# Optimization experiments

Measured on AMD Instinct MI355X. Metric: run time of the kernel, lower is better.

## Reference

```python
import jax, jax.numpy as jnp
import numpy as np

N = 50000      # nodes
E = 800000     # directed edges
GNN_DIM = 128  # node feature dim
HID = 64       # per-head hidden dim of conv1
HEADS = 2
OUT = 16       # output_dim (classes)
TEXT = 500     # tf-idf text dim
M = 10000      # masked / labeled nodes


def setup_inputs() -> dict:
    key = jax.random.key(0)
    ks = jax.random.split(key, 32)
    w = lambda k, s: jax.random.normal(k, s, jnp.float32) * 0.05
    inp = {
        'text_features': jax.random.normal(ks[0], (M, TEXT), jnp.float32),
        'x': jax.random.normal(ks[1], (N, GNN_DIM), jnp.float32),
        'edge_index': jax.random.randint(ks[2], (2, E), 0, N),
        'mask': jax.random.randint(ks[3], (M,), 0, N),
        # text MLP (Linear stored as [in, out])
        'fc1_w': w(ks[4], (TEXT, 128)), 'fc1_b': w(ks[5], (128,)),
        'fc2_w': w(ks[6], (128, 64)),  'fc2_b': w(ks[7], (64,)),
        'fc3_w': w(ks[8], (64, 16)),   'fc3_b': w(ks[9], (16,)),
        'fc4_w': w(ks[10], (16, OUT)), 'fc4_b': w(ks[11], (OUT,)),
        'sc_w': w(ks[12], (TEXT, OUT)), 'sc_b': w(ks[13], (OUT,)),
        # GATConv1: in=GNN_DIM, heads=2, out=HID, concat=True
        'W1': w(ks[14], (GNN_DIM, HEADS * HID)),
        'att_src1': w(ks[15], (HEADS, HID)), 'att_dst1': w(ks[16], (HEADS, HID)),
        'b1': w(ks[17], (HEADS * HID,)),
        # GATConv2: in=2*HID, heads=1, out=OUT, concat=False
        'W2': w(ks[18], (HEADS * HID, OUT)),
        'att_src2': w(ks[19], (1, OUT)), 'att_dst2': w(ks[20], (1, OUT)),
        'b2': w(ks[21], (OUT,)),
        # fc_final: [2*OUT, OUT]
        'fcf_w': w(ks[22], (2 * OUT, OUT)), 'fcf_b': w(ks[23], (OUT,)),
    }
    return inp


def _gat_layer(h_in, src, dst, W, a_src, a_dst, b, heads, dim, concat):
    # PyG GATConv (default negative_slope=0.2, self-loops already appended)
    n = h_in.shape[0]
    h = (h_in @ W).reshape(n, heads, dim)                      # [N,H,D]
    a_s = jnp.einsum('nhd,hd->nh', h, a_src)                   # [N,H]
    a_d = jnp.einsum('nhd,hd->nh', h, a_dst)
    e = jax.nn.leaky_relu(a_s[src] + a_d[dst], 0.2)            # [E,H]
    emax = jax.ops.segment_max(e, dst, num_segments=n)
    ex = jnp.exp(e - emax[dst])
    den = jax.ops.segment_sum(ex, dst, num_segments=n)
    alpha = ex / (den[dst] + 1e-16)                            # [E,H]
    msg = h[src] * alpha[:, :, None]                           # [E,H,D]
    out = jax.ops.segment_sum(msg, dst, num_segments=n)        # [N,H,D]
    out = out.reshape(n, heads * dim) if concat else out.mean(axis=1)
    return out + b


def reference(text_features, x, edge_index, mask,
              fc1_w, fc1_b, fc2_w, fc2_b, fc3_w, fc3_b, fc4_w, fc4_b,
              sc_w, sc_b, W1, att_src1, att_dst1, b1,
              W2, att_src2, att_dst2, b2, fcf_w, fcf_b):
    n = x.shape[0]
    loop = jnp.arange(n, dtype=edge_index.dtype)
    src = jnp.concatenate([edge_index[0], loop])
    dst = jnp.concatenate([edge_index[1], loop])

    # GNN branch
    g = jax.nn.relu(_gat_layer(x, src, dst, W1, att_src1, att_dst1, b1,
                               HEADS, HID, True))
    g = _gat_layer(g, src, dst, W2, att_src2, att_dst2, b2, 1, OUT, False)
    gnn_out = g[mask]                                          # [M,OUT]

    # text MLP branch with shortcut
    t = jax.nn.relu(text_features @ fc1_w + fc1_b)
    t = jax.nn.relu(t @ fc2_w + fc2_b)
    t = jax.nn.relu(t @ fc3_w + fc3_b)
    text_out = (t @ fc4_w + fc4_b) + (text_features @ sc_w + sc_b)  # [M,OUT]

    combined = jnp.concatenate([text_out, gnn_out], axis=1)    # [M,2*OUT]
    return jax.nn.log_softmax(combined @ fcf_w + fcf_b, axis=1)
```

## Files before the change

kernel.cpp:

```cpp
#include <hip/hip_runtime.h>
#include <hip/hip_bf16.h>
#include <cmath>

#define TEXTD 500
#define GNN_DIM 128
#define DEGP(v) ((v) << 5)

typedef __attribute__((ext_vector_type(8))) short bf16x8;
typedef __attribute__((ext_vector_type(4))) float f32x4;

__device__ __forceinline__ float bf2f(unsigned short u) {
    union { unsigned int i; float f; } cv;
    cv.i = ((unsigned int)u) << 16;
    return cv.f;
}
__device__ __forceinline__ unsigned short f2b(float x) {
    __hip_bfloat16 b = __float2bfloat16(x);
    return *reinterpret_cast<unsigned short*>(&b);
}
__device__ __forceinline__ float u2f(unsigned int u) {
    union { unsigned int i; float f; } cv; cv.i = u; return cv.f;
}
__device__ __forceinline__ bf16x8 cvt8(const float* p) {
    float4 u = *(const float4*)p;
    float4 v = *(const float4*)(p + 4);
    bf16x8 f;
    f[0] = (short)f2b(u.x); f[1] = (short)f2b(u.y);
    f[2] = (short)f2b(u.z); f[3] = (short)f2b(u.w);
    f[4] = (short)f2b(v.x); f[5] = (short)f2b(v.y);
    f[6] = (short)f2b(v.z); f[7] = (short)f2b(v.w);
    return f;
}

__global__ __launch_bounds__(256) void setup_kernel(
    int* __restrict__ deg, int N, int NB,
    const float* __restrict__ fc1_w, const float* __restrict__ sc_w,
    const float* __restrict__ W1, const float* __restrict__ W2,
    const float* __restrict__ fc2_w, const float* __restrict__ fc3_w,
    const float* __restrict__ fc4_w,
    unsigned short* __restrict__ w1cat, unsigned short* __restrict__ w1g,
    unsigned short* __restrict__ w2t, unsigned short* __restrict__ fc2t,
    unsigned short* __restrict__ fc3t, unsigned short* __restrict__ fc4t)
{
    if ((int)blockIdx.x < NB) {
        int v = blockIdx.x * 256 + threadIdx.x;
        if (v < N) deg[DEGP(v)] = 0;
        return;
    }
    int idx = (blockIdx.x - NB) * 256 + threadIdx.x;
    if (idx < 73728) {
        int n = idx >> 9, k = idx & 511;
        float v = 0.f;
        if (k < TEXTD) v = (n < 128) ? fc1_w[k * 128 + n] : sc_w[k * 16 + (n - 128)];
        w1cat[idx] = f2b(v);
    } else if (idx < 90112) {
        int j = idx - 73728;
        int n = j >> 7, k = j & 127;
        w1g[j] = f2b(W1[k * 128 + n]);
    } else if (idx < 92160) {
        int j = idx - 90112;
        int n = j >> 7, k = j & 127;
        w2t[j] = f2b(W2[k * 16 + n]);
    } else if (idx < 100352) {
        int j = idx - 92160;
        int n = j >> 7, k = j & 127;
        fc2t[j] = f2b(fc2_w[k * 64 + n]);
    } else if (idx < 101376) {
        int j = idx - 100352;
        int n = j >> 6, k = j & 63;
        fc3t[j] = f2b(fc3_w[k * 16 + n]);
    } else if (idx < 101888) {
        int j = idx - 101376;
        int n = j >> 5, k = j & 31;
        fc4t[j] = f2b((k < 16) ? fc4_w[k * 16 + n] : 0.f);
    }
}

__global__ __launch_bounds__(64) void text_mfma_kernel(
    const float* __restrict__ text, const short* __restrict__ w1cat,
    const float* __restrict__ fc1_b, const float* __restrict__ sc_b,
    const short* __restrict__ fc2t, const float* __restrict__ fc2_b,
    const short* __restrict__ fc3t, const float* __restrict__ fc3_b,
    const short* __restrict__ fc4t, const float* __restrict__ fc4_b,
    float* __restrict__ text_out, int M)
{
    __shared__ unsigned short t1b[16 * 136];
    __shared__ unsigned short t2b[16 * 72];
    __shared__ unsigned short t3b[16 * 40];
    __shared__ float tscs[16 * 16];

    const int lane = threadIdx.x;
    const int q = lane >> 4, col = lane & 15;
    const int mb = blockIdx.x * 16;
    const int arow = min(mb + col, M - 1);
    const float* ap = text + (size_t)arow * TEXTD + q * 8;

    bf16x8 afrag[16];
    #pragma unroll
    for (int ks = 0; ks < 15; ks++) afrag[ks] = cvt8(ap + ks * 32);
    {
        bf16x8 f;
        int k0 = 480 + q * 8;
        #pragma unroll
        for (int e = 0; e < 8; e++) {
            int k = k0 + e;
            f[e] = (short)((k < TEXTD) ? f2b(text[(size_t)arow * TEXTD + k]) : 0);
        }
        afrag[15] = f;
    }

    for (int nb = 0; nb < 9; nb++) {
        const short* bp = w1cat + (size_t)(nb * 16 + col) * 512 + q * 8;
        f32x4 acc = {0.f, 0.f, 0.f, 0.f};
        #pragma unroll
        for (int ks = 0; ks < 16; ks++)
            acc = __builtin_amdgcn_mfma_f32_16x16x32_bf16(afrag[ks], *(const bf16x8*)(bp + ks * 32), acc, 0, 0, 0);
        #pragma unroll
        for (int i = 0; i < 4; i++) {
            int row = q * 4 + i;
            if (nb < 8) t1b[row * 136 + nb * 16 + col] = f2b(fmaxf(acc[i] + fc1_b[nb * 16 + col], 0.f));
            else        tscs[row * 16 + col] = acc[i] + sc_b[col];
        }
    }
    __syncthreads();

    const unsigned short* a2p = t1b + col * 136 + q * 8;
    #pragma unroll
    for (int nt = 0; nt < 4; nt++) {
        const short* bp = fc2t + (nt * 16 + col) * 128 + q * 8;
        f32x4 acc = {0.f, 0.f, 0.f, 0.f};
        #pragma unroll
        for (int ks = 0; ks < 4; ks++)
            acc = __builtin_amdgcn_mfma_f32_16x16x32_bf16(
                *(const bf16x8*)(a2p + ks * 32), *(const bf16x8*)(bp + ks * 32), acc, 0, 0, 0);
        #pragma unroll
        for (int i = 0; i < 4; i++) {
            int row = q * 4 + i;
            t2b[row * 72 + nt * 16 + col] = f2b(fmaxf(acc[i] + fc2_b[nt * 16 + col], 0.f));
        }
    }
    __syncthreads();

    {
        const unsigned short* a3p = t2b + col * 72 + q * 8;
        const short* bp = fc3t + col * 64 + q * 8;
        f32x4 acc = {0.f, 0.f, 0.f, 0.f};
        #pragma unroll
        for (int ks = 0; ks < 2; ks++)
            acc = __builtin_amdgcn_mfma_f32_16x16x32_bf16(
                *(const bf16x8*)(a3p + ks * 32), *(const bf16x8*)(bp + ks * 32), acc, 0, 0, 0);
        #pragma unroll
        for (int i = 0; i < 4; i++) {
            int row = q * 4 + i;
            t3b[row * 40 + col] = f2b(fmaxf(acc[i] + fc3_b[col], 0.f));
            t3b[row * 40 + 16 + col] = 0;
        }
    }
    __syncthreads();

    {
        const unsigned short* a4p = t3b + col * 40 + q * 8;
        const short* bp = fc4t + col * 32 + q * 8;
        f32x4 acc = {0.f, 0.f, 0.f, 0.f};
        acc = __builtin_amdgcn_mfma_f32_16x16x32_bf16(
            *(const bf16x8*)a4p, *(const bf16x8*)bp, acc, 0, 0, 0);
        #pragma unroll
        for (int i = 0; i < 4; i++) {
            int row = q * 4 + i;
            int rg = mb + row;
            if (rg < M) text_out[(size_t)rg * 16 + col] = acc[i] + fc4_b[col] + tscs[row * 16 + col];
        }
    }
}

__global__ __launch_bounds__(256) void gemm_h1_kernel(
    const float* __restrict__ x, const short* __restrict__ B,
    const float* __restrict__ as1w, const float* __restrict__ ad1w,
    unsigned short* __restrict__ h1, float* __restrict__ a_s, float* __restrict__ a_d, int N)
{
    const int tid = threadIdx.x;
    const int wave = tid >> 6, lane = tid & 63;
    const int q = lane >> 4, col = lane & 15;
    const int mb = blockIdx.x * 64 + wave * 16;
    const int arow = min(mb + col, N - 1);
    const float* ap = x + (size_t)arow * 128 + q * 8;

    bf16x8 afrag[4];
    #pragma unroll
    for (int ks = 0; ks < 4; ks++) afrag[ks] = cvt8(ap + ks * 32);

    float ps0[4] = {0,0,0,0}, ps1[4] = {0,0,0,0};
    float pd0[4] = {0,0,0,0}, pd1[4] = {0,0,0,0};

    #pragma unroll
    for (int nb = 0; nb < 8; nb++) {
        const short* bp = B + (size_t)(nb * 16 + col) * 128 + q * 8;
        f32x4 acc = {0.f, 0.f, 0.f, 0.f};
        #pragma unroll
        for (int ks = 0; ks < 4; ks++)
            acc = __builtin_amdgcn_mfma_f32_16x16x32_bf16(afrag[ks], *(const bf16x8*)(bp + ks * 32), acc, 0, 0, 0);
        const int j = nb * 16 + col;
        const float asj = as1w[j], adj = ad1w[j];
        #pragma unroll
        for (int i = 0; i < 4; i++) {
            int row = mb + q * 4 + i;
            if (row < N) h1[(size_t)row * 128 + j] = f2b(acc[i]);
            if (nb < 4) { ps0[i] = fmaf(acc[i], asj, ps0[i]); pd0[i] = fmaf(acc[i], adj, pd0[i]); }
            else        { ps1[i] = fmaf(acc[i], asj, ps1[i]); pd1[i] = fmaf(acc[i], adj, pd1[i]); }
        }
    }
    #pragma unroll
    for (int i = 0; i < 4; i++) {
        float v0 = ps0[i], v1 = ps1[i], w0 = pd0[i], w1 = pd1[i];
        #pragma unroll
        for (int off = 1; off < 16; off <<= 1) {
            v0 += __shfl_xor(v0, off, 16);
            v1 += __shfl_xor(v1, off, 16);
            w0 += __shfl_xor(w0, off, 16);
            w1 += __shfl_xor(w1, off, 16);
        }
        int row = mb + q * 4 + i;
        if (col == 0 && row < N) {
            a_s[2 * row] = v0; a_s[2 * row + 1] = v1;
            a_d[2 * row] = w0; a_d[2 * row + 1] = w1;
        }
    }
}

__global__ __launch_bounds__(256) void deg_hist_kernel(
    const int* __restrict__ edst, int* __restrict__ deg, int* __restrict__ rank, int E)
{
    const int base = blockIdx.x * 1024 + threadIdx.x;
    int e0 = base;
    int e1 = base + 256;
    int e2 = base + 512;
    int e3 = base + 768;
    int d0 = (e0 < E) ? edst[e0] : -1;
    int d1 = (e1 < E) ? edst[e1] : -1;
    int d2 = (e2 < E) ? edst[e2] : -1;
    int d3 = (e3 < E) ? edst[e3] : -1;
    int r0 = (d0 >= 0) ? atomicAdd(&deg[DEGP(d0)], 1) : 0;
    int r1 = (d1 >= 0) ? atomicAdd(&deg[DEGP(d1)], 1) : 0;
    int r2 = (d2 >= 0) ? atomicAdd(&deg[DEGP(d2)], 1) : 0;
    int r3 = (d3 >= 0) ? atomicAdd(&deg[DEGP(d3)], 1) : 0;
    if (d0 >= 0) rank[e0] = r0;
    if (d1 >= 0) rank[e1] = r1;
    if (d2 >= 0) rank[e2] = r2;
    if (d3 >= 0) rank[e3] = r3;
}

__global__ __launch_bounds__(256) void part_kernel(
    const int* __restrict__ deg, int* __restrict__ bsum, int N)
{
    const int tid = threadIdx.x;
    int i = blockIdx.x * 256 + tid;
    int d = (i < N) ? deg[DEGP(i)] + 1 : 0;
    #pragma unroll
    for (int off = 32; off > 0; off >>= 1) d += __shfl_down(d, off, 64);
    __shared__ int wsum[4];
    if ((tid & 63) == 0) wsum[tid >> 6] = d;
    __syncthreads();
    if (tid == 0) bsum[blockIdx.x] = wsum[0] + wsum[1] + wsum[2] + wsum[3];
}

__global__ __launch_bounds__(256) void rowptr_kernel(
    const int* __restrict__ deg, const int* __restrict__ bsum,
    int* __restrict__ rowptr, int N, int NB)
{
    __shared__ int bsc[256];
    __shared__ int sc[256];
    const int tid = threadIdx.x;

    int bv = (tid < NB) ? bsum[tid] : 0;
    bsc[tid] = bv;
    for (int off = 1; off < 256; off <<= 1) {
        __syncthreads();
        int t = (tid >= off) ? bsc[tid - off] : 0;
        __syncthreads();
        bsc[tid] += t;
    }
    __syncthreads();
    const int base = (blockIdx.x == 0) ? 0 : bsc[blockIdx.x - 1];

    const int i = blockIdx.x * 256 + tid;
    int d = (i < N) ? deg[DEGP(i)] + 1 : 0;
    sc[tid] = d;
    for (int off = 1; off < 256; off <<= 1) {
        __syncthreads();
        int t = (tid >= off) ? sc[tid - off] : 0;
        __syncthreads();
        sc[tid] += t;
    }
    __syncthreads();
    int incl = sc[tid];
    if (i < N) rowptr[i] = base + incl - d;
    if (i == N - 1) rowptr[N] = base + incl;
}

__device__ __forceinline__ float edge_w(float e) {
    return __expf(e > 0.f ? e : 0.2f * e);
}

__global__ __launch_bounds__(256) void fillw_kernel(
    const int* __restrict__ esrc, const int* __restrict__ edst,
    const int* __restrict__ rank, const int* __restrict__ rowptr,
    uint2* __restrict__ eslot,
    const float* __restrict__ a_s, const float* __restrict__ a_d, int E, int N)
{
    int e = blockIdx.x * 256 + threadIdx.x;
    if (e < E) {
        int src = esrc[e], dst = edst[e];
        int pos = rowptr[dst] + 1 + rank[e];
        float2 as = *(const float2*)(a_s + 2 * src);
        float2 ad = *(const float2*)(a_d + 2 * dst);
        unsigned int w0 = f2b(edge_w(as.x + ad.x));
        unsigned int w1 = f2b(edge_w(as.y + ad.y));
        uint2 o; o.x = (unsigned int)src; o.y = (w1 << 16) | w0;
        eslot[pos] = o;
    } else if (e < E + N) {
        int v = e - E;
        float2 as = *(const float2*)(a_s + 2 * v);
        float2 ad = *(const float2*)(a_d + 2 * v);
        unsigned int w0 = f2b(edge_w(as.x + ad.x));
        unsigned int w1 = f2b(edge_w(as.y + ad.y));
        uint2 o; o.x = (unsigned int)v; o.y = (w1 << 16) | w0;
        eslot[rowptr[v]] = o;
    }
}

template<int B>
__device__ __forceinline__ void gat1_batch(
    int i0, int end, int endm1, int wsh,
    const uint2* __restrict__ eslot, const uint2* __restrict__ h1u, unsigned int dp,
    float& a0, float& a1, float& a2, float& a3, float& den)
{
    int ics[B];
    uint2 sl[B];
    float wv[B];
    uint2 hv[B];
    #pragma unroll
    for (int k = 0; k < B; k++) ics[k] = min(i0 + 2 * k, endm1);
    #pragma unroll
    for (int k = 0; k < B; k++) sl[k] = eslot[ics[k]];
    #pragma unroll
    for (int k = 0; k < B; k++) {
        float w = u2f((sl[k].y << wsh) & 0xffff0000u);
        wv[k] = (i0 + 2 * k < end) ? w : 0.f;
    }
    #pragma unroll
    for (int k = 0; k < B; k++) hv[k] = h1u[(sl[k].x << 5) | dp];
    #pragma unroll
    for (int k = 0; k < B; k++) {
        float w = wv[k];
        den += w;
        a0 = fmaf(w, u2f(hv[k].x << 16),          a0);
        a1 = fmaf(w, u2f(hv[k].x & 0xffff0000u),  a1);
        a2 = fmaf(w, u2f(hv[k].y << 16),          a2);
        a3 = fmaf(w, u2f(hv[k].y & 0xffff0000u),  a3);
    }
}

__global__ __launch_bounds__(256) void gat1_gather_kernel(
    const int* __restrict__ rowptr, const uint2* __restrict__ eslot,
    const uint2* __restrict__ h1u,
    const float* __restrict__ b1, uint2* __restrict__ g1b, int N)
{
    const int v = blockIdx.x * 4 + (threadIdx.x >> 6);
    if (v >= N) return;
    const int lane = threadIdx.x & 63;
    const int slot = lane >> 5;
    const unsigned int dp = lane & 31;
    const int head = dp >> 4;
    const int wsh = head ? 0 : 16;
    const int beg = rowptr[v], end = rowptr[v + 1];
    const int deg = end - beg;
    const int endm1 = end - 1;
    const int i0 = beg + slot;

    float a0 = 0.f, a1 = 0.f, a2 = 0.f, a3 = 0.f, den = 0.f;

    if (deg <= 8) {
        gat1_batch<4>(i0, end, endm1, wsh, eslot, h1u, dp, a0, a1, a2, a3, den);
    } else {
        gat1_batch<8>(i0, end, endm1, wsh, eslot, h1u, dp, a0, a1, a2, a3, den);
        for (int base = i0 + 16; base < end; base += 8)
            gat1_batch<4>(base, end, endm1, wsh, eslot, h1u, dp, a0, a1, a2, a3, den);
    }

    a0 += __shfl_xor(a0, 32, 64);
    a1 += __shfl_xor(a1, 32, 64);
    a2 += __shfl_xor(a2, 32, 64);
    a3 += __shfl_xor(a3, 32, 64);
    den += __shfl_xor(den, 32, 64);

    if (lane < 32) {
        float inv = 1.f / (den + 1e-16f);
        float4 bv = *(const float4*)(b1 + 4 * dp);
        float o0 = fmaxf(fmaf(a0, inv, bv.x), 0.f);
        float o1 = fmaxf(fmaf(a1, inv, bv.y), 0.f);
        float o2 = fmaxf(fmaf(a2, inv, bv.z), 0.f);
        float o3 = fmaxf(fmaf(a3, inv, bv.w), 0.f);
        uint2 o;
        o.x = ((unsigned int)f2b(o1) << 16) | f2b(o0);
        o.y = ((unsigned int)f2b(o3) << 16) | f2b(o2);
        g1b[((unsigned int)v << 5) | dp] = o;
    }
}

__global__ __launch_bounds__(256) void gat2_proj_kernel(
    const unsigned short* __restrict__ g1b, const short* __restrict__ w2t,
    const float* __restrict__ as2w, const float* __restrict__ ad2w,
    float* __restrict__ h2, float* __restrict__ a_s2, float* __restrict__ a_d2, int N)
{
    const int tid = threadIdx.x;
    const int wave = tid >> 6, lane = tid & 63;
    const int q = lane >> 4, col = lane & 15;
    const int mb = blockIdx.x * 64 + wave * 16;
    const int arow = min(mb + col, N - 1);
    const short* ap = (const short*)g1b + (size_t)arow * 128 + q * 8;
    const short* bp = w2t + (size_t)col * 128 + q * 8;

    f32x4 acc = {0.f, 0.f, 0.f, 0.f};
    #pragma unroll
    for (int ks = 0; ks < 4; ks++)
        acc = __builtin_amdgcn_mfma_f32_16x16x32_bf16(
            *(const bf16x8*)(ap + ks * 32), *(const bf16x8*)(bp + ks * 32), acc, 0, 0, 0);

    const float asj = as2w[col], adj = ad2w[col];
    #pragma unroll
    for (int i = 0; i < 4; i++) {
        int row = mb + q * 4 + i;
        float ps = acc[i] * asj, pd = acc[i] * adj;
        #pragma unroll
        for (int off = 1; off < 16; off <<= 1) {
            ps += __shfl_xor(ps, off, 16);
            pd += __shfl_xor(pd, off, 16);
        }
        if (row < N) {
            h2[(size_t)row * 16 + col] = acc[i];
            if (col == 0) { a_s2[row] = ps; a_d2[row] = pd; }
        }
    }
}

__global__ __launch_bounds__(256) void gat2_final_kernel(
    const int* __restrict__ rowptr, const uint2* __restrict__ eslot,
    const float* __restrict__ h2,
    const float* __restrict__ a_s2, const float* __restrict__ a_d2,
    const float* __restrict__ b2, const int* __restrict__ mask,
    const float* __restrict__ text_out,
    const float* __restrict__ fcf_w, const float* __restrict__ fcf_b,
    float* __restrict__ out, int M)
{
    const int tid = threadIdx.x;
    const int m = blockIdx.x * 4 + (tid >> 6);
    if (m >= M) return;
    const int lane = tid & 63, slot = lane >> 4, c = lane & 15;
    const int v = mask[m];
    const float adv = a_d2[v];
    const int beg = rowptr[v], end = rowptr[v + 1];
    const int i0 = beg + slot;

    float acc = 0.f, den = 0.f;
    unsigned int idxs[8];
    float msk[8], as_[8], hval[8];
    #pragma unroll
    for (int k = 0; k < 8; k++) {
        int i = i0 + 4 * k;
        int ic = min(i, end - 1);
        idxs[k] = eslot[ic].x;
        msk[k] = (i < end) ? 1.f : 0.f;
    }
    #pragma unroll
    for (int k = 0; k < 8; k++) as_[k] = a_s2[idxs[k]];
    #pragma unroll
    for (int k = 0; k < 8; k++) hval[k] = h2[(idxs[k] << 4) | (unsigned)c];
    #pragma unroll
    for (int k = 0; k < 8; k++) {
        float e = as_[k] + adv;
        float w = msk[k] * __expf(e > 0.f ? e : 0.2f * e);
        den += w;
        acc = fmaf(w, hval[k], acc);
    }
    for (int i = i0 + 32; i < end; i += 4) {
        unsigned int src = eslot[i].x;
        float e = a_s2[src] + adv;
        float w = __expf(e > 0.f ? e : 0.2f * e);
        den += w;
        acc = fmaf(w, h2[(src << 4) | (unsigned)c], acc);
    }

    acc += __shfl_xor(acc, 16, 64);
    acc += __shfl_xor(acc, 32, 64);
    den += __shfl_xor(den, 16, 64);
    den += __shfl_xor(den, 32, 64);

    if (slot == 0) {
        float gval = acc / (den + 1e-16f) + b2[c];
        float tval = text_out[(size_t)m * 16 + c];

        float logit = fcf_b[c];
        #pragma unroll
        for (int k = 0; k < 16; k++) {
            logit = fmaf(__shfl(tval, k, 16), fcf_w[k * 16 + c], logit);
            logit = fmaf(__shfl(gval, k, 16), fcf_w[(16 + k) * 16 + c], logit);
        }
        float mx = logit;
        #pragma unroll
        for (int off = 8; off > 0; off >>= 1) mx = fmaxf(mx, __shfl_xor(mx, off, 16));
        float se = expf(logit - mx);
        #pragma unroll
        for (int off = 8; off > 0; off >>= 1) se += __shfl_xor(se, off, 16);
        out[(size_t)m * 16 + c] = logit - mx - logf(se);
    }
}

extern "C" void kernel_launch(void* const* d_in, const int* in_sizes, int n_in,
                              void* d_out, int out_size, void* d_ws, size_t ws_size,
                              hipStream_t stream)
{
    const float* text  = (const float*)d_in[0];
    const float* x     = (const float*)d_in[1];
    const int*   ei    = (const int*)  d_in[2];
    const int*   mask  = (const int*)  d_in[3];
    const float* fc1_w = (const float*)d_in[4];  const float* fc1_b = (const float*)d_in[5];
    const float* fc2_w = (const float*)d_in[6];  const float* fc2_b = (const float*)d_in[7];
    const float* fc3_w = (const float*)d_in[8];  const float* fc3_b = (const float*)d_in[9];
    const float* fc4_w = (const float*)d_in[10]; const float* fc4_b = (const float*)d_in[11];
    const float* sc_w  = (const float*)d_in[12]; const float* sc_b  = (const float*)d_in[13];
    const float* W1    = (const float*)d_in[14];
    const float* as1w  = (const float*)d_in[15]; const float* ad1w  = (const float*)d_in[16];
    const float* b1    = (const float*)d_in[17];
    const float* W2    = (const float*)d_in[18];
    const float* as2w  = (const float*)d_in[19]; const float* ad2w  = (const float*)d_in[20];
    const float* b2    = (const float*)d_in[21];
    const float* fcf_w = (const float*)d_in[22]; const float* fcf_b = (const float*)d_in[23];

    const int M  = in_sizes[3];
    const int N  = in_sizes[1] / GNN_DIM;
    const int E  = in_sizes[2] / 2;
    const int EP = E + N;
    const int* esrc = ei;
    const int* edst = ei + E;

    const int Np = ((N + 63) / 64) * 64;
    const int NB = (N + 255) / 256;

    float* ws = (float*)d_ws;
    size_t off = 0;
    auto alloc = [&](size_t n) { float* p = ws + off; off += (n + 63) & ~size_t(63); return p; };

    unsigned short* h1    = (unsigned short*)alloc((size_t)Np * 64);
    unsigned int*   g1b   = (unsigned int*)  alloc((size_t)N * 64);
    unsigned short* w1cat = (unsigned short*)alloc(144 * 256);
    unsigned short* w1g   = (unsigned short*)alloc(128 * 64);
    unsigned short* w2t   = (unsigned short*)alloc(16 * 64);
    unsigned short* fc2t  = (unsigned short*)alloc(64 * 64);
    unsigned short* fc3t  = (unsigned short*)alloc(16 * 32);
    unsigned short* fc4t  = (unsigned short*)alloc(16 * 16);
    float* a_s1     = alloc((size_t)2 * N);
    float* a_d1     = alloc((size_t)2 * N);
    float* h2       = alloc((size_t)N * 16);
    float* a_s2     = alloc(N);
    float* a_d2     = alloc(N);
    float* text_out = alloc((size_t)M * 16);
    uint2* eslot    = (uint2*)alloc((size_t)2 * EP);
    int* deg        = (int*)alloc((size_t)N * 32);
    int* rank       = (int*)alloc(E);
    int* rowptr     = (int*)alloc(N + 1);
    int* bsum       = (int*)alloc(256);

    const int convBlocks = (101888 + 255) / 256;

    setup_kernel<<<NB + convBlocks, 256, 0, stream>>>(
        deg, N, NB, fc1_w, sc_w, W1, W2, fc2_w, fc3_w, fc4_w,
        w1cat, w1g, w2t, fc2t, fc3t, fc4t);

    deg_hist_kernel<<<(E + 1023) / 1024, 256, 0, stream>>>(edst, deg, rank, E);
    part_kernel<<<NB, 256, 0, stream>>>(deg, bsum, N);
    rowptr_kernel<<<NB, 256, 0, stream>>>(deg, bsum, rowptr, N, NB);

    gemm_h1_kernel<<<Np / 64, 256, 0, stream>>>(
        x, (const short*)w1g, as1w, ad1w, h1, a_s1, a_d1, N);

    fillw_kernel<<<(E + N + 255) / 256, 256, 0, stream>>>(
        esrc, edst, rank, rowptr, eslot, a_s1, a_d1, E, N);

    text_mfma_kernel<<<(M + 15) / 16, 64, 0, stream>>>(
        text, (const short*)w1cat, fc1_b, sc_b,
        (const short*)fc2t, fc2_b, (const short*)fc3t, fc3_b,
        (const short*)fc4t, fc4_b, text_out, M);

    gat1_gather_kernel<<<(N + 3) / 4, 256, 0, stream>>>(
        rowptr, eslot, (const uint2*)h1, b1, (uint2*)g1b, N);

    gat2_proj_kernel<<<Np / 64, 256, 0, stream>>>(
        (const unsigned short*)g1b, (const short*)w2t, as2w, ad2w, h2, a_s2, a_d2, N);

    gat2_final_kernel<<<(M + 3) / 4, 256, 0, stream>>>(
        rowptr, eslot, h2, a_s2, a_d2, b2, mask, text_out, fcf_w, fcf_b,
        (float*)d_out, M);
}
```

Before: 182.0 us.

## Split text MLP first-layer K dimension across four waves with LDS reduction

The text MLP kernel moves from one wave per 16-row tile to four waves. Each wave computes a partial product over a 128-wide slice of the 500-dim input, and the partials are reduced through shared memory. The fc2 layer is then split across waves by output tile, while fc3 and fc4 run on wave 0 only. This cuts per-wave register pressure and serial MFMA chain length, and adds a large LDS partial buffer (about 36KB per block) plus extra barriers, which may limit occupancy.

```diff
diff --git a/kernel.cpp b/kernel.cpp
--- a/kernel.cpp
+++ b/kernel.cpp
@@ -76,7 +76,7 @@
     }
 }
 
-__global__ __launch_bounds__(64) void text_mfma_kernel(
+__global__ __launch_bounds__(256) void text_mfma_kernel(
     const float* __restrict__ text, const short* __restrict__ w1cat,
     const float* __restrict__ fc1_b, const float* __restrict__ sc_b,
     const short* __restrict__ fc2t, const float* __restrict__ fc2_b,
@@ -84,50 +84,70 @@
     const short* __restrict__ fc4t, const float* __restrict__ fc4_b,
     float* __restrict__ text_out, int M)
 {
+    __shared__ float part[4 * 9 * 256];
     __shared__ unsigned short t1b[16 * 136];
     __shared__ unsigned short t2b[16 * 72];
     __shared__ unsigned short t3b[16 * 40];
     __shared__ float tscs[16 * 16];
 
-    const int lane = threadIdx.x;
+    const int tid = threadIdx.x;
+    const int w = tid >> 6, lane = tid & 63;
     const int q = lane >> 4, col = lane & 15;
     const int mb = blockIdx.x * 16;
     const int arow = min(mb + col, M - 1);
-    const float* ap = text + (size_t)arow * TEXTD + q * 8;
-
-    bf16x8 afrag[16];
-    #pragma unroll
-    for (int ks = 0; ks < 15; ks++) afrag[ks] = cvt8(ap + ks * 32);
+    const int kofs = w * 128;
+
+    bf16x8 afrag[4];
+    #pragma unroll
+    for (int ks = 0; ks < 4; ks++) {
+        int k0 = kofs + ks * 32 + q * 8;
+        if (k0 + 7 < TEXTD) {
+            afrag[ks] = cvt8(text + (size_t)arow * TEXTD + k0);
+        } else {
+            bf16x8 f;
+            #pragma unroll
+            for (int e = 0; e < 8; e++) {
+                int k = k0 + e;
+                f[e] = (short)((k < TEXTD) ? f2b(text[(size_t)arow * TEXTD + k]) : 0);
+            }
+            afrag[ks] = f;
+        }
+    }
+
+    for (int nb = 0; nb < 9; nb++) {
+        const short* bp = w1cat + (size_t)(nb * 16 + col) * 512 + kofs + q * 8;
+        f32x4 acc = {0.f, 0.f, 0.f, 0.f};
+        #pragma unroll
+        for (int ks = 0; ks < 4; ks++)
+            acc = __builtin_amdgcn_mfma_f32_16x16x32_bf16(afrag[ks], *(const bf16x8*)(bp + ks * 32), acc, 0, 0, 0);
+        #pragma unroll
+        for (int i = 0; i < 4; i++)
+            part[w * 2304 + nb * 256 + i * 64 + lane] = acc[i];
+    }
+    __syncthreads();
+
     {
-        bf16x8 f;
-        int k0 = 480 + q * 8;
-        #pragma unroll
-        for (int e = 0; e < 8; e++) {
-            int k = k0 + e;
-            f[e] = (short)((k < TEXTD) ? f2b(text[(size_t)arow * TEXTD + k]) : 0);
-        }
-        afrag[15] = f;
-    }
-
-    for (int nb = 0; nb < 9; nb++) {
-        const short* bp = w1cat + (size_t)(nb * 16 + col) * 512 + q * 8;
-        f32x4 acc = {0.f, 0.f, 0.f, 0.f};
-        #pragma unroll
-        for (int ks = 0; ks < 16; ks++)
-            acc = __builtin_amdgcn_mfma_f32_16x16x32_bf16(afrag[ks], *(const bf16x8*)(bp + ks * 32), acc, 0, 0, 0);
-        #pragma unroll
-        for (int i = 0; i < 4; i++) {
-            int row = q * 4 + i;
-            if (nb < 8) t1b[row * 136 + nb * 16 + col] = f2b(fmaxf(acc[i] + fc1_b[nb * 16 + col], 0.f));
-            else        tscs[row * 16 + col] = acc[i] + sc_b[col];
+        int nb0 = w * 2;
+        int cnt = (w == 3) ? 3 : 2;
+        for (int t = 0; t < cnt; t++) {
+            int nb = nb0 + t;
+            #pragma unroll
+            for (int i = 0; i < 4; i++) {
+                float a = part[nb * 256 + i * 64 + lane]
+                        + part[2304 + nb * 256 + i * 64 + lane]
+                        + part[4608 + nb * 256 + i * 64 + lane]
+                        + part[6912 + nb * 256 + i * 64 + lane];
+                int row = q * 4 + i;
+                if (nb < 8) t1b[row * 136 + nb * 16 + col] = f2b(fmaxf(a + fc1_b[nb * 16 + col], 0.f));
+                else        tscs[row * 16 + col] = a + sc_b[col];
+            }
         }
     }
     __syncthreads();
 
-    const unsigned short* a2p = t1b + col * 136 + q * 8;
-    #pragma unroll
-    for (int nt = 0; nt < 4; nt++) {
-        const short* bp = fc2t + (nt * 16 + col) * 128 + q * 8;
+    {
+        const unsigned short* a2p = t1b + col * 136 + q * 8;
+        const short* bp = fc2t + (w * 16 + col) * 128 + q * 8;
         f32x4 acc = {0.f, 0.f, 0.f, 0.f};
         #pragma unroll
         for (int ks = 0; ks < 4; ks++)
@@ -136,39 +156,39 @@
         #pragma unroll
         for (int i = 0; i < 4; i++) {
             int row = q * 4 + i;
-            t2b[row * 72 + nt * 16 + col] = f2b(fmaxf(acc[i] + fc2_b[nt * 16 + col], 0.f));
+            t2b[row * 72 + w * 16 + col] = f2b(fmaxf(acc[i] + fc2_b[w * 16 + col], 0.f));
         }
     }
     __syncthreads();
 
-    {
-        const unsigned short* a3p = t2b + col * 72 + q * 8;
-        const short* bp = fc3t + col * 64 + q * 8;
-        f32x4 acc = {0.f, 0.f, 0.f, 0.f};
-        #pragma unroll
-        for (int ks = 0; ks < 2; ks++)
+    if (w == 0) {
+        {
+            const unsigned short* a3p = t2b + col * 72 + q * 8;
+            const short* bp = fc3t + col * 64 + q * 8;
+            f32x4 acc = {0.f, 0.f, 0.f, 0.f};
+            #pragma unroll
+            for (int ks = 0; ks < 2; ks++)
+                acc = __builtin_amdgcn_mfma_f32_16x16x32_bf16(
+                    *(const bf16x8*)(a3p + ks * 32), *(const bf16x8*)(bp + ks * 32), acc, 0, 0, 0);
+            #pragma unroll
+            for (int i = 0; i < 4; i++) {
+                int row = q * 4 + i;
+                t3b[row * 40 + col] = f2b(fmaxf(acc[i] + fc3_b[col], 0.f));
+                t3b[row * 40 + 16 + col] = 0;
+            }
+        }
+        {
+            const unsigned short* a4p = t3b + col * 40 + q * 8;
+            const short* bp = fc4t + col * 32 + q * 8;
+            f32x4 acc = {0.f, 0.f, 0.f, 0.f};
             acc = __builtin_amdgcn_mfma_f32_16x16x32_bf16(
-                *(const bf16x8*)(a3p + ks * 32), *(const bf16x8*)(bp + ks * 32), acc, 0, 0, 0);
-        #pragma unroll
-        for (int i = 0; i < 4; i++) {
-            int row = q * 4 + i;
-            t3b[row * 40 + col] = f2b(fmaxf(acc[i] + fc3_b[col], 0.f));
-            t3b[row * 40 + 16 + col] = 0;
-        }
-    }
-    __syncthreads();
-
-    {
-        const unsigned short* a4p = t3b + col * 40 + q * 8;
-        const short* bp = fc4t + col * 32 + q * 8;
-        f32x4 acc = {0.f, 0.f, 0.f, 0.f};
-        acc = __builtin_amdgcn_mfma_f32_16x16x32_bf16(
-            *(const bf16x8*)a4p, *(const bf16x8*)bp, acc, 0, 0, 0);
-        #pragma unroll
-        for (int i = 0; i < 4; i++) {
-            int row = q * 4 + i;
-            int rg = mb + row;
-            if (rg < M) text_out[(size_t)rg * 16 + col] = acc[i] + fc4_b[col] + tscs[row * 16 + col];
+                *(const bf16x8*)a4p, *(const bf16x8*)bp, acc, 0, 0, 0);
+            #pragma unroll
+            for (int i = 0; i < 4; i++) {
+                int row = q * 4 + i;
+                int rg = mb + row;
+                if (rg < M) text_out[(size_t)rg * 16 + col] = acc[i] + fc4_b[col] + tscs[row * 16 + col];
+            }
         }
     }
 }
@@ -586,7 +606,7 @@
     fillw_kernel<<<(E + N + 255) / 256, 256, 0, stream>>>(
         esrc, edst, rank, rowptr, eslot, a_s1, a_d1, E, N);
 
-    text_mfma_kernel<<<(M + 15) / 16, 64, 0, stream>>>(
+    text_mfma_kernel<<<(M + 15) / 16, 256, 0, stream>>>(
         text, (const short*)w1cat, fc1_b, sc_b,
         (const short*)fc2t, fc2_b, (const short*)fc3t, fc3_b,
         (const short*)fc4t, fc4_b, text_out, M);
```

New measurement: 164.9 us, median of 2. 9.4% less time.
